# Kernel tuning notes

Measured on AMD Instinct MI355X. Metric: run time of the kernel, lower is better.

The kernel has to match this reference:

```python
import jax, jax.numpy as jnp
import numpy as np

B, T, INPUT_DIM = 4, 2048, 1024
DIM, H = 64, 16  # per-head dim, n_heads


def setup_inputs() -> dict:
    key = jax.random.key(0)
    k1, k2, k3, k4 = jax.random.split(key, 4)
    x = jax.random.normal(k1, (B, T, INPUT_DIM), dtype=jnp.float32)
    # nn.Linear(input_dim, 3*h*d, bias=False)
    w_qkv = jax.random.normal(k2, (INPUT_DIM, 3 * H * DIM), dtype=jnp.float32) * (INPUT_DIM ** -0.5)
    # nn.Linear(h*d, input_dim) with bias
    w_out = jax.random.normal(k3, (H * DIM, INPUT_DIM), dtype=jnp.float32) * ((H * DIM) ** -0.5)
    b_out = jax.random.normal(k4, (INPUT_DIM,), dtype=jnp.float32) * 0.01
    return {"x": x, "w_qkv": w_qkv, "w_out": w_out, "b_out": b_out}


def reference(x, w_qkv, w_out, b_out):
    b, t, _ = x.shape
    scale = DIM ** -0.5
    qkv = x @ w_qkv                                   # [b, t, 3*h*d]
    # 'b t (qkv h d) -> qkv b h t d'
    qkv = qkv.reshape(b, t, 3, H, DIM)
    qkv = jnp.transpose(qkv, (2, 0, 3, 1, 4))         # [3, b, h, t, d]
    q, k, v = qkv[0], qkv[1], qkv[2]
    dot = jnp.einsum('bhtd,bhkd->bhtk', q, k) * scale # [b, h, t, t]
    att = jax.nn.softmax(dot, axis=-1)
    out = jnp.einsum('bhtk,bhkd->bhtd', att, v)       # [b, h, t, d]
    out = jnp.transpose(out, (0, 2, 1, 3)).reshape(b, t, H * DIM)
    return out @ w_out + b_out
```

## Files before the change

### kernel.cpp

```cpp
#include <hip/hip_runtime.h>
#include <hip/hip_bf16.h>
#include <stdint.h>

typedef __attribute__((ext_vector_type(8))) short bf16x8;
typedef __attribute__((ext_vector_type(4))) short s16x4;
typedef __attribute__((ext_vector_type(4))) float f32x4;
typedef __attribute__((ext_vector_type(16))) float f32x16;

__device__ __forceinline__ void mfma_bf16(f32x4& c, bf16x8 a, bf16x8 b) {
  asm("v_mfma_f32_16x16x32_bf16 %0, %1, %2, %0" : "+v"(c) : "v"(a), "v"(b));
}
__device__ __forceinline__ void mfma32_bf16(f32x16& c, bf16x8 a, bf16x8 b) {
  asm("v_mfma_f32_32x32x16_bf16 %0, %1, %2, %0" : "+v"(c) : "v"(a), "v"(b));
}

__device__ __forceinline__ void gload_lds16(const void* g, void* lds) {
  __builtin_amdgcn_global_load_lds(
      (const __attribute__((address_space(1))) void*)g,
      (__attribute__((address_space(3))) void*)lds, 16, 0, 0);
}

__global__ void cvt_f32_bf16(const float* __restrict__ in, __hip_bfloat16* __restrict__ out, int n4) {
  int i = blockIdx.x * blockDim.x + threadIdx.x;
  if (i >= n4) return;
  float4 v = reinterpret_cast<const float4*>(in)[i];
  __hip_bfloat162 a = __float22bfloat162_rn(make_float2(v.x, v.y));
  __hip_bfloat162 b = __float22bfloat162_rn(make_float2(v.z, v.w));
  reinterpret_cast<__hip_bfloat162*>(out)[i * 2]     = a;
  reinterpret_cast<__hip_bfloat162*>(out)[i * 2 + 1] = b;
}

__global__ void transpose_cvt(const float* __restrict__ in, __hip_bfloat16* __restrict__ out,
                              int R, int C) {
  __shared__ float tile[32][33];
  int c0 = blockIdx.x * 32, r0 = blockIdx.y * 32;
#pragma unroll
  for (int k = 0; k < 4; k++)
    tile[threadIdx.y + 8 * k][threadIdx.x] =
        in[(size_t)(r0 + threadIdx.y + 8 * k) * C + c0 + threadIdx.x];
  __syncthreads();
#pragma unroll
  for (int k = 0; k < 4; k++)
    out[(size_t)(c0 + threadIdx.y + 8 * k) * R + r0 + threadIdx.x] =
        __float2bfloat16(tile[threadIdx.x][threadIdx.y + 8 * k]);
}

template <int MODE>
__global__ __launch_bounds__(256) void gemm_bf16(
    const __hip_bfloat16* __restrict__ A, const __hip_bfloat16* __restrict__ Bt,
    int M, int N, int K,
    __hip_bfloat16* __restrict__ qb, __hip_bfloat16* __restrict__ kb,
    __hip_bfloat16* __restrict__ vt,
    float* __restrict__ outp, const float* __restrict__ bias) {
  constexpr int BK = 32;
  __shared__ __align__(16) __hip_bfloat16 As[128 * BK];
  __shared__ __align__(16) __hip_bfloat16 Bs[128 * BK];
  const int tid = threadIdx.x;
  const int wave = tid >> 6, lane = tid & 63;
  const int wr = wave >> 1, wc = wave & 1;
  const int m0 = blockIdx.y * 128;
  const int n0 = (MODE == 2 ? 2048 : 0) + blockIdx.x * 128;

  f32x4 acc[4][4];
#pragma unroll
  for (int i = 0; i < 4; i++)
#pragma unroll
    for (int j = 0; j < 4; j++) acc[i][j] = (f32x4)(0.0f);

  const int c0 = wave * 2, c1 = c0 + 1;
  const int srow0 = c0 * 16 + (lane >> 2);
  const int srow1 = c1 * 16 + (lane >> 2);
  const int scol = (lane & 3) * 8;
  const __hip_bfloat16* Ag0 = A + (size_t)(m0 + srow0) * K + scol;
  const __hip_bfloat16* Ag1 = A + (size_t)(m0 + srow1) * K + scol;
  const __hip_bfloat16* Bg0 = Bt + (size_t)(n0 + srow0) * K + scol;
  const __hip_bfloat16* Bg1 = Bt + (size_t)(n0 + srow1) * K + scol;
  __hip_bfloat16* AsP0 = &As[c0 * 512];
  __hip_bfloat16* AsP1 = &As[c1 * 512];
  __hip_bfloat16* BsP0 = &Bs[c0 * 512];
  __hip_bfloat16* BsP1 = &Bs[c1 * 512];

  for (int kk = 0; kk < K; kk += BK) {
    gload_lds16(Ag0 + kk, AsP0);
    gload_lds16(Ag1 + kk, AsP1);
    gload_lds16(Bg0 + kk, BsP0);
    gload_lds16(Bg1 + kk, BsP1);
    __syncthreads();
    bf16x8 af[4], bfr[4];
#pragma unroll
    for (int i = 0; i < 4; i++)
      af[i] = *(const bf16x8*)&As[(wr * 64 + i * 16 + (lane & 15)) * BK + (lane >> 4) * 8];
#pragma unroll
    for (int j = 0; j < 4; j++)
      bfr[j] = *(const bf16x8*)&Bs[(wc * 64 + j * 16 + (lane & 15)) * BK + (lane >> 4) * 8];
#pragma unroll
    for (int i = 0; i < 4; i++)
#pragma unroll
      for (int j = 0; j < 4; j++) {
        if constexpr (MODE == 2)
          mfma_bf16(acc[i][j], bfr[j], af[i]);
        else
          mfma_bf16(acc[i][j], af[i], bfr[j]);
      }
    __syncthreads();
  }

  if constexpr (MODE == 0) {
#pragma unroll
    for (int j = 0; j < 4; j++) {
      int col = n0 + wc * 64 + j * 16 + (lane & 15);
      int sel = col >> 10;
      int h = (col >> 6) & 15;
      int d = col & 63;
      __hip_bfloat16* dst = sel ? kb : qb;
      float scl = sel ? 1.0f : 0.18033688f;
#pragma unroll
      for (int i = 0; i < 4; i++) {
#pragma unroll
        for (int r = 0; r < 4; r++) {
          int row = m0 + wr * 64 + i * 16 + (lane >> 4) * 4 + r;
          int b = row >> 11, t = row & 2047;
          dst[(((size_t)b * 16 + h) * 2048 + t) * 64 + d] = __float2bfloat16(acc[i][j][r] * scl);
        }
      }
    }
  } else if constexpr (MODE == 2) {
#pragma unroll
    for (int j = 0; j < 4; j++) {
#pragma unroll
      for (int r = 0; r < 4; r++) {
        int nrow = n0 + wc * 64 + j * 16 + (lane >> 4) * 4 + r;
        int h = (nrow >> 6) & 15;
        int d = nrow & 63;
#pragma unroll
        for (int i = 0; i < 4; i++) {
          int tcol = m0 + wr * 64 + i * 16 + (lane & 15);
          int b = tcol >> 11, t = tcol & 2047;
          vt[(((size_t)b * 16 + h) * 64 + d) * 2048 + t] = __float2bfloat16(acc[i][j][r]);
        }
      }
    }
  } else {
#pragma unroll
    for (int j = 0; j < 4; j++) {
      int col = n0 + wc * 64 + j * 16 + (lane & 15);
      float bv = bias[col];
#pragma unroll
      for (int i = 0; i < 4; i++) {
#pragma unroll
        for (int r = 0; r < 4; r++) {
          int row = m0 + wr * 64 + i * 16 + (lane >> 4) * 4 + r;
          outp[(size_t)row * N + col] = acc[i][j][r] + bv;
        }
      }
    }
  }
}

__global__ __launch_bounds__(256) void attn_fwd(
    const __hip_bfloat16* __restrict__ Qb, const __hip_bfloat16* __restrict__ Kb,
    const __hip_bfloat16* __restrict__ Vtg, __hip_bfloat16* __restrict__ Ob) {
  constexpr int T = 2048;
  constexpr float THR = 11.5f;
  __shared__ __align__(16) __hip_bfloat16 Ks[2][4096];
  __shared__ __align__(16) __hip_bfloat16 Vs[2][4096];
  const int tid = threadIdx.x, wave = tid >> 6, lane = tid & 63;

  int id = ((int)blockIdx.x & 7) * 128 + ((int)blockIdx.x >> 3);
  const int bh = id >> 4, q0 = (id & 15) * 128;
  const size_t baseQ = (size_t)bh * T * 64;
  const size_t baseV = (size_t)bh * 64 * T;
  const int l31 = lane & 31, half = lane >> 5;

  bf16x8 qf[4];
  const int qrow = q0 + wave * 32 + l31;
#pragma unroll
  for (int ks = 0; ks < 4; ks++)
    qf[ks] = *(const bf16x8*)&Qb[baseQ + (size_t)qrow * 64 + ks * 16 + half * 8];

  float m_run = -3.0e38f;
  float l_part = 0.0f;
  f32x16 o0 = (f32x16)(0.0f), o1 = (f32x16)(0.0f);

  const int sr = lane >> 3;
  const int q8 = (lane & 7) ^ sr;
  const char* KgB = (const char*)(Kb + baseQ);
  const char* VgB = (const char*)(Vtg + baseV);
  const int cc0 = wave * 2, cc1 = cc0 + 1;
  const int swz = (l31 & 7) << 4;

#define STAGE(kt, buf)                                                                        \
  do {                                                                                        \
    char* kd = (char*)Ks[buf];                                                                \
    char* vd = (char*)Vs[buf];                                                                \
    gload_lds16(KgB + (size_t)((kt) * 64 + cc0 * 8 + sr) * 128 + q8 * 16, kd + cc0 * 1024);   \
    gload_lds16(KgB + (size_t)((kt) * 64 + cc1 * 8 + sr) * 128 + q8 * 16, kd + cc1 * 1024);   \
    gload_lds16(VgB + (size_t)(cc0 * 8 + sr) * 4096 + (kt) * 128 + q8 * 16, vd + cc0 * 1024); \
    gload_lds16(VgB + (size_t)(cc1 * 8 + sr) * 4096 + (kt) * 128 + q8 * 16, vd + cc1 * 1024); \
  } while (0)

  STAGE(0, 0);
  int cur = 0;

  for (int kt = 0; kt < T / 64; kt++) {
    if (kt < T / 64 - 1) {
      STAGE(kt + 1, cur ^ 1);
      asm volatile("s_waitcnt vmcnt(4)" ::: "memory");
    } else {
      asm volatile("s_waitcnt vmcnt(0)" ::: "memory");
    }
    __builtin_amdgcn_s_barrier();
    __builtin_amdgcn_sched_barrier(0);
    const char* KsB = (const char*)Ks[cur];
    const char* VtB = (const char*)Vs[cur];

    f32x16 s0 = (f32x16)(0.0f), s1 = (f32x16)(0.0f);
    __builtin_amdgcn_s_setprio(1);
#pragma unroll
    for (int ks = 0; ks < 4; ks++) {
      bf16x8 kf0 = *(const bf16x8*)(KsB + ((l31 * 128 + ks * 32 + half * 16) ^ swz));
      bf16x8 kf1 = *(const bf16x8*)(KsB + (((32 + l31) * 128 + ks * 32 + half * 16) ^ swz));
      mfma32_bf16(s0, kf0, qf[ks]);
      mfma32_bf16(s1, kf1, qf[ks]);
    }
    __builtin_amdgcn_s_setprio(0);

    float mx[8];
#pragma unroll
    for (int i = 0; i < 8; i++)
      mx[i] = fmaxf(fmaxf(s0[2 * i], s0[2 * i + 1]), fmaxf(s1[2 * i], s1[2 * i + 1]));
    float tm = fmaxf(fmaxf(fmaxf(mx[0], mx[1]), fmaxf(mx[2], mx[3])),
                     fmaxf(fmaxf(mx[4], mx[5]), fmaxf(mx[6], mx[7])));
    tm = fmaxf(tm, __shfl_xor(tm, 32));

    if (!__all(tm - m_run <= THR)) {
      float mn = fmaxf(m_run, tm);
      float alpha = __builtin_exp2f(m_run - mn);
      m_run = mn;
      l_part *= alpha;
#pragma unroll
      for (int r = 0; r < 16; r++) {
        o0[r] *= alpha;
        o1[r] *= alpha;
      }
    }

    float rs0 = 0.0f, rs1 = 0.0f;
#pragma unroll
    for (int r = 0; r < 16; r++) {
      s0[r] = __builtin_exp2f(s0[r] - m_run);
      s1[r] = __builtin_exp2f(s1[r] - m_run);
      rs0 += s0[r];
      rs1 += s1[r];
    }
    l_part += rs0 + rs1;

    __builtin_amdgcn_s_setprio(1);
#pragma unroll
    for (int kb = 0; kb < 2; kb++) {
      int cw[8];
#pragma unroll
      for (int m = 0; m < 8; m++) {
        float pa = (kb == 0) ? s0[2 * m] : s1[2 * m];
        float pb = (kb == 0) ? s0[2 * m + 1] : s1[2 * m + 1];
        __hip_bfloat162 h2 = __float22bfloat162_rn(make_float2(pa, pb));
        cw[m] = *(int*)&h2;
      }
      asm("v_permlane32_swap_b32 %0, %1" : "+v"(cw[0]), "+v"(cw[2]));
      asm("v_permlane32_swap_b32 %0, %1" : "+v"(cw[1]), "+v"(cw[3]));
      asm("v_permlane32_swap_b32 %0, %1" : "+v"(cw[4]), "+v"(cw[6]));
      asm("v_permlane32_swap_b32 %0, %1" : "+v"(cw[5]), "+v"(cw[7]));
      int4 w0 = make_int4(cw[0], cw[1], cw[2], cw[3]);
      int4 w1 = make_int4(cw[4], cw[5], cw[6], cw[7]);
      bf16x8 pb0 = *(bf16x8*)&w0;
      bf16x8 pb1 = *(bf16x8*)&w1;
      bf16x8 va0 = *(const bf16x8*)(VtB + ((l31 * 128 + kb * 64 + half * 16) ^ swz));
      bf16x8 vb0 = *(const bf16x8*)(VtB + (((32 + l31) * 128 + kb * 64 + half * 16) ^ swz));
      bf16x8 va1 = *(const bf16x8*)(VtB + ((l31 * 128 + kb * 64 + 32 + half * 16) ^ swz));
      bf16x8 vb1 = *(const bf16x8*)(VtB + (((32 + l31) * 128 + kb * 64 + 32 + half * 16) ^ swz));
      mfma32_bf16(o0, va0, pb0);
      mfma32_bf16(o1, vb0, pb0);
      mfma32_bf16(o0, va1, pb1);
      mfma32_bf16(o1, vb1, pb1);
    }
    __builtin_amdgcn_s_setprio(0);
    __builtin_amdgcn_sched_barrier(0);
    __builtin_amdgcn_s_barrier();
    cur ^= 1;
  }
#undef STAGE

  float l_run = l_part + __shfl_xor(l_part, 32);
  float inv = 1.0f / l_run;
  const int b = bh >> 4, h = bh & 15;
  const int trow = q0 + wave * 32 + l31;
  __hip_bfloat16* orow = Ob + ((size_t)(b * 2048 + trow)) * 1024 + h * 64;
#pragma unroll
  for (int db = 0; db < 2; db++) {
#pragma unroll
    for (int rq = 0; rq < 4; rq++) {
      int d0 = db * 32 + rq * 8 + half * 4;
      s16x4 w;
#pragma unroll
      for (int e = 0; e < 4; e++) {
        float val = (db == 0 ? o0[rq * 4 + e] : o1[rq * 4 + e]) * inv;
        w[e] = (short)__bfloat16_as_short(__float2bfloat16(val));
      }
      *(s16x4*)(orow + d0) = w;
    }
  }
}

extern "C" void kernel_launch(void* const* d_in, const int* in_sizes, int n_in,
                              void* d_out, int out_size, void* d_ws, size_t ws_size,
                              hipStream_t stream) {
  const float* x = (const float*)d_in[0];
  const float* w_qkv = (const float*)d_in[1];
  const float* w_out = (const float*)d_in[2];
  const float* b_out = (const float*)d_in[3];
  float* out = (float*)d_out;

  size_t need = (size_t)37748736 * 2;
  if (ws_size < need) return;
  __hip_bfloat16* wsp = (__hip_bfloat16*)d_ws;
  __hip_bfloat16* x_bf = wsp;
  __hip_bfloat16* wqkv_t = x_bf + 8192 * 1024;
  __hip_bfloat16* wout_t = wqkv_t + 3072 * 1024;
  __hip_bfloat16* qb = wout_t + 1024 * 1024;
  __hip_bfloat16* kb = qb + 8388608;
  __hip_bfloat16* vt = kb + 8388608;
  __hip_bfloat16* ab = x_bf;

  cvt_f32_bf16<<<8192, 256, 0, stream>>>(x, x_bf, 8192 * 1024 / 4);
  transpose_cvt<<<dim3(3072 / 32, 1024 / 32), dim3(32, 8), 0, stream>>>(w_qkv, wqkv_t, 1024, 3072);
  transpose_cvt<<<dim3(1024 / 32, 1024 / 32), dim3(32, 8), 0, stream>>>(w_out, wout_t, 1024, 1024);
  gemm_bf16<0><<<dim3(16, 64), 256, 0, stream>>>(x_bf, wqkv_t, 8192, 3072, 1024,
                                                 qb, kb, nullptr, nullptr, nullptr);
  gemm_bf16<2><<<dim3(8, 64), 256, 0, stream>>>(x_bf, wqkv_t, 8192, 3072, 1024,
                                                nullptr, nullptr, vt, nullptr, nullptr);
  attn_fwd<<<1024, 256, 0, stream>>>(qb, kb, vt, ab);
  gemm_bf16<1><<<dim3(8, 64), 256, 0, stream>>>(ab, wout_t, 8192, 1024, 1024,
                                                nullptr, nullptr, nullptr, out, b_out);
}
```

Before: 248.5 us.

## Use 512-thread attention blocks with 256 query rows and fold max into MFMA init

The attention kernel now runs 8 waves per block covering 256 query rows, so every K/V tile staged in LDS is shared by twice as many queries. Each wave issues one K and one V load per tile instead of two each, which halves global/LDS traffic per query. Separately, the running max is pre-subtracted by seeding the score accumulators with -m_run, so the per-element subtraction before exp2 disappears and the rescale path only subtracts the delta. The risk is higher register pressure under launch_bounds(512,4) and fewer blocks in the grid, which can hurt tail balance. The change to a running max starting at 0 also alters numerics slightly.

```diff
diff --git a/kernel.cpp b/kernel.cpp
--- a/kernel.cpp
+++ b/kernel.cpp
@@ -157,7 +157,7 @@
   }
 }
 
-__global__ __launch_bounds__(256) void attn_fwd(
+__global__ __launch_bounds__(512, 4) void attn_fwd(
     const __hip_bfloat16* __restrict__ Qb, const __hip_bfloat16* __restrict__ Kb,
     const __hip_bfloat16* __restrict__ Vtg, __hip_bfloat16* __restrict__ Ob) {
   constexpr int T = 2048;
@@ -166,8 +166,8 @@
   __shared__ __align__(16) __hip_bfloat16 Vs[2][4096];
   const int tid = threadIdx.x, wave = tid >> 6, lane = tid & 63;
 
-  int id = ((int)blockIdx.x & 7) * 128 + ((int)blockIdx.x >> 3);
-  const int bh = id >> 4, q0 = (id & 15) * 128;
+  int id = ((int)blockIdx.x & 7) * 64 + ((int)blockIdx.x >> 3);
+  const int bh = id >> 3, q0 = (id & 7) * 256;
   const size_t baseQ = (size_t)bh * T * 64;
   const size_t baseV = (size_t)bh * 64 * T;
   const int l31 = lane & 31, half = lane >> 5;
@@ -178,7 +178,7 @@
   for (int ks = 0; ks < 4; ks++)
     qf[ks] = *(const bf16x8*)&Qb[baseQ + (size_t)qrow * 64 + ks * 16 + half * 8];
 
-  float m_run = -3.0e38f;
+  float m_run = 0.0f;
   float l_part = 0.0f;
   f32x16 o0 = (f32x16)(0.0f), o1 = (f32x16)(0.0f);
 
@@ -186,17 +186,14 @@
   const int q8 = (lane & 7) ^ sr;
   const char* KgB = (const char*)(Kb + baseQ);
   const char* VgB = (const char*)(Vtg + baseV);
-  const int cc0 = wave * 2, cc1 = cc0 + 1;
   const int swz = (l31 & 7) << 4;
 
-#define STAGE(kt, buf)                                                                        \
-  do {                                                                                        \
-    char* kd = (char*)Ks[buf];                                                                \
-    char* vd = (char*)Vs[buf];                                                                \
-    gload_lds16(KgB + (size_t)((kt) * 64 + cc0 * 8 + sr) * 128 + q8 * 16, kd + cc0 * 1024);   \
-    gload_lds16(KgB + (size_t)((kt) * 64 + cc1 * 8 + sr) * 128 + q8 * 16, kd + cc1 * 1024);   \
-    gload_lds16(VgB + (size_t)(cc0 * 8 + sr) * 4096 + (kt) * 128 + q8 * 16, vd + cc0 * 1024); \
-    gload_lds16(VgB + (size_t)(cc1 * 8 + sr) * 4096 + (kt) * 128 + q8 * 16, vd + cc1 * 1024); \
+#define STAGE(kt, buf)                                                                          \
+  do {                                                                                          \
+    char* kd = (char*)Ks[buf];                                                                  \
+    char* vd = (char*)Vs[buf];                                                                  \
+    gload_lds16(KgB + (size_t)((kt) * 64 + wave * 8 + sr) * 128 + q8 * 16, kd + wave * 1024);   \
+    gload_lds16(VgB + (size_t)(wave * 8 + sr) * 4096 + (kt) * 128 + q8 * 16, vd + wave * 1024); \
   } while (0)
 
   STAGE(0, 0);
@@ -205,7 +202,7 @@
   for (int kt = 0; kt < T / 64; kt++) {
     if (kt < T / 64 - 1) {
       STAGE(kt + 1, cur ^ 1);
-      asm volatile("s_waitcnt vmcnt(4)" ::: "memory");
+      asm volatile("s_waitcnt vmcnt(2)" ::: "memory");
     } else {
       asm volatile("s_waitcnt vmcnt(0)" ::: "memory");
     }
@@ -214,7 +211,12 @@
     const char* KsB = (const char*)Ks[cur];
     const char* VtB = (const char*)Vs[cur];
 
-    f32x16 s0 = (f32x16)(0.0f), s1 = (f32x16)(0.0f);
+    f32x16 s0, s1;
+#pragma unroll
+    for (int r = 0; r < 16; r++) {
+      s0[r] = -m_run;
+      s1[r] = -m_run;
+    }
     __builtin_amdgcn_s_setprio(1);
 #pragma unroll
     for (int ks = 0; ks < 4; ks++) {
@@ -233,13 +235,15 @@
                      fmaxf(fmaxf(mx[4], mx[5]), fmaxf(mx[6], mx[7])));
     tm = fmaxf(tm, __shfl_xor(tm, 32));
 
-    if (!__all(tm - m_run <= THR)) {
-      float mn = fmaxf(m_run, tm);
-      float alpha = __builtin_exp2f(m_run - mn);
-      m_run = mn;
+    if (!__all(tm <= THR)) {
+      float d = fmaxf(tm, 0.0f);
+      float alpha = __builtin_exp2f(-d);
+      m_run += d;
       l_part *= alpha;
 #pragma unroll
       for (int r = 0; r < 16; r++) {
+        s0[r] -= d;
+        s1[r] -= d;
         o0[r] *= alpha;
         o1[r] *= alpha;
       }
@@ -248,8 +252,8 @@
     float rs0 = 0.0f, rs1 = 0.0f;
 #pragma unroll
     for (int r = 0; r < 16; r++) {
-      s0[r] = __builtin_exp2f(s0[r] - m_run);
-      s1[r] = __builtin_exp2f(s1[r] - m_run);
+      s0[r] = __builtin_exp2f(s0[r]);
+      s1[r] = __builtin_exp2f(s1[r]);
       rs0 += s0[r];
       rs1 += s1[r];
     }
@@ -338,7 +342,7 @@
                                                  qb, kb, nullptr, nullptr, nullptr);
   gemm_bf16<2><<<dim3(8, 64), 256, 0, stream>>>(x_bf, wqkv_t, 8192, 3072, 1024,
                                                 nullptr, nullptr, vt, nullptr, nullptr);
-  attn_fwd<<<1024, 256, 0, stream>>>(qb, kb, vt, ab);
+  attn_fwd<<<512, 512, 0, stream>>>(qb, kb, vt, ab);
   gemm_bf16<1><<<dim3(8, 64), 256, 0, stream>>>(ab, wout_t, 8192, 1024, 1024,
                                                 nullptr, nullptr, nullptr, out, b_out);
 }
```

New measurement: 236.3 us. 4.9% less time.
